# Kernel tuning notes

Measured on AMD Instinct MI355X. Metric: run time of the kernel, lower is better.

## Reference

```python
import jax, jax.numpy as jnp
import numpy as np

N = 50000       # nodes
E = 800000      # random edges (self-loops appended in reference)
F_IN = 3        # dataset.num_features
CH = 32         # conv_hidden_channels
HEADS = 4       # attention_heads
C1_OUT = CH * 2     # 64
C2_OUT = CH * 4     # 128
LIN = 256       # lin_hidden_channels
NCLS = 25       # dataset.num_classes


def setup_inputs() -> dict:
    key = jax.random.key(0)
    ks = jax.random.split(key, 20)
    g = lambda k, s: (jax.random.normal(k, s, jnp.float32) * 0.05)
    return {
        "x": jax.random.normal(ks[0], (N, F_IN), jnp.float32),
        "edge_index": jax.random.randint(ks[1], (2, E), 0, N, dtype=jnp.int64),
        # fc0 (Linear stored as [in, out])
        "fc0_w": g(ks[2], (F_IN, CH)), "fc0_b": g(ks[3], (CH,)),
        # FeaStConv 1: in=CH, out=C1_OUT
        "conv1_w": g(ks[4], (CH, HEADS * C1_OUT)),
        "conv1_u": g(ks[5], (CH, HEADS)),
        "conv1_c": g(ks[6], (HEADS,)),
        "conv1_b": g(ks[7], (C1_OUT,)),
        # FeaStConv 2: in=C1_OUT, out=C2_OUT
        "conv2_w": g(ks[8], (C1_OUT, HEADS * C2_OUT)),
        "conv2_u": g(ks[9], (C1_OUT, HEADS)),
        "conv2_c": g(ks[10], (HEADS,)),
        "conv2_b": g(ks[11], (C2_OUT,)),
        # fc1, fc2
        "fc1_w": g(ks[12], (C2_OUT, LIN)), "fc1_b": g(ks[13], (LIN,)),
        "fc2_w": g(ks[14], (LIN, NCLS)), "fc2_b": g(ks[15], (NCLS,)),
    }


def feast_conv(x, src, dst, W, u, c, b):
    """FeaStConv (PyG): q = softmax((x_j - x_i) u + c) over heads,
    msg = sum_h q_h * (x_j W_h), mean-aggregated onto dst nodes."""
    xi = x[dst]                          # [E', in]
    xj = x[src]                          # [E', in]
    q = jax.nn.softmax((xj - xi) @ u + c, axis=-1)   # [E', H]
    m = (xj @ W).reshape(xj.shape[0], HEADS, -1)     # [E', H, out]
    msg = jnp.einsum('eh,ehd->ed', q, m)             # [E', out]
    agg = jax.ops.segment_sum(msg, dst, num_segments=N)
    cnt = jax.ops.segment_sum(jnp.ones((msg.shape[0],), x.dtype), dst,
                              num_segments=N)
    return agg / cnt[:, None] + b


def reference(x, edge_index, fc0_w, fc0_b,
              conv1_w, conv1_u, conv1_c, conv1_b,
              conv2_w, conv2_u, conv2_c, conv2_b,
              fc1_w, fc1_b, fc2_w, fc2_b):
    loops = jnp.arange(N, dtype=edge_index.dtype)
    src = jnp.concatenate([edge_index[0], loops])   # messages flow src -> dst
    dst = jnp.concatenate([edge_index[1], loops])
    h = jax.nn.elu(x @ fc0_w + fc0_b)
    h = jax.nn.elu(feast_conv(h, src, dst, conv1_w, conv1_u, conv1_c, conv1_b))
    h = jax.nn.elu(feast_conv(h, src, dst, conv2_w, conv2_u, conv2_c, conv2_b))
    h = jax.nn.elu(h @ fc1_w + fc1_b)
    # dropout skipped (eval mode / training=self.training)
    out = h @ fc2_w + fc2_b
    return jax.nn.log_softmax(out, axis=1)
```

## Files before the change

kernel.cpp:

```cpp
#include <hip/hip_runtime.h>
#include <math.h>

#define F_IN 3
#define CH 32
#define HEADS 4
#define C1_OUT 64
#define C2_OUT 128
#define LIN 256
#define NCLS 25
#define NBIN 8

typedef __attribute__((ext_vector_type(8))) short bf16x8;
typedef __attribute__((ext_vector_type(4))) float f32x4;

__device__ __forceinline__ float elu_f(float x) {
    return x > 0.f ? x : (__expf(x) - 1.f);
}

__device__ __forceinline__ unsigned short f2bf(float f) {
    union { float f; unsigned int u; } v; v.f = f;
    unsigned int u = v.u + 0x7fffu + ((v.u >> 16) & 1u);
    return (unsigned short)(u >> 16);
}

__device__ __forceinline__ float bf2f(unsigned short u) {
    union { unsigned int u; float f; } v; v.u = ((unsigned int)u) << 16;
    return v.f;
}

__device__ __forceinline__ void unpackq(unsigned lo, unsigned hi, float& x, float& y,
                                        float& z, float& w) {
    x = bf2f((unsigned short)(lo & 0xffffu));
    y = bf2f((unsigned short)(lo >> 16));
    z = bf2f((unsigned short)(hi & 0xffffu));
    w = bf2f((unsigned short)(hi >> 16));
}

__device__ __forceinline__ void softmax4(const float* __restrict__ c,
                                         float& q0, float& q1, float& q2, float& q3) {
    float c0 = c[0], c1 = c[1], c2 = c[2], c3 = c[3];
    float mx = fmaxf(fmaxf(c0, c1), fmaxf(c2, c3));
    float e0 = __expf(c0 - mx), e1 = __expf(c1 - mx);
    float e2 = __expf(c2 - mx), e3 = __expf(c3 - mx);
    float inv = 1.f / (e0 + e1 + e2 + e3);
    q0 = e0 * inv; q1 = e1 * inv; q2 = e2 * inv; q3 = e3 * inv;
}

__device__ __forceinline__ void qslot(const float4* __restrict__ pp, float4 pd,
                                      float c0, float c1, float c2, float c3,
                                      int sx, bool valid,
                                      unsigned& qlo, unsigned& qhi) {
    float4 ps = pp[sx];
    float t0 = ps.x - pd.x + c0;
    float t1 = ps.y - pd.y + c1;
    float t2 = ps.z - pd.z + c2;
    float t3 = ps.w - pd.w + c3;
    float mx = fmaxf(fmaxf(t0, t1), fmaxf(t2, t3));
    float s0 = __expf(t0 - mx), s1 = __expf(t1 - mx);
    float s2 = __expf(t2 - mx), s3 = __expf(t3 - mx);
    float inv = 1.f / (s0 + s1 + s2 + s3);
    qlo = qhi = 0u;
    if (valid) {
        qlo = (unsigned)f2bf(s0 * inv) | ((unsigned)f2bf(s1 * inv) << 16);
        qhi = (unsigned)f2bf(s2 * inv) | ((unsigned)f2bf(s3 * inv) << 16);
    }
}

__global__ __launch_bounds__(256) void k_fc0(
    const float* __restrict__ x, const float* __restrict__ w,
    const float* __restrict__ b, const float* __restrict__ u,
    unsigned short* __restrict__ h0, float* __restrict__ p, int n_nodes) {
    int wid = (blockIdx.x * blockDim.x + threadIdx.x) >> 6;
    int lane = threadIdx.x & 63;
    int half = lane >> 5, c = lane & 31;
    int node = wid * 2 + half;
    if (node >= n_nodes) return;
    float acc = b[c];
#pragma unroll
    for (int i = 0; i < F_IN; ++i) acc += x[node * F_IN + i] * w[i * CH + c];
    unsigned short hb = f2bf(elu_f(acc));
    h0[(size_t)node * CH + c] = hb;
    float hv = bf2f(hb);
    float a0 = hv * u[c * HEADS + 0];
    float a1 = hv * u[c * HEADS + 1];
    float a2 = hv * u[c * HEADS + 2];
    float a3 = hv * u[c * HEADS + 3];
#pragma unroll
    for (int m = 16; m >= 1; m >>= 1) {
        a0 += __shfl_xor(a0, m, 32); a1 += __shfl_xor(a1, m, 32);
        a2 += __shfl_xor(a2, m, 32); a3 += __shfl_xor(a3, m, 32);
    }
    if (c == 0) {
        p[node * 4 + 0] = a0; p[node * 4 + 1] = a1;
        p[node * 4 + 2] = a2; p[node * 4 + 3] = a3;
    }
}

__global__ void k_deg(const int* __restrict__ dst, int* __restrict__ deg,
                      int ne, int npb) {
    int bin = blockIdx.x & (NBIN - 1);
    int blk = blockIdx.x >> 3;
    int nblk = gridDim.x >> 3;
    int per = (ne + nblk - 1) / nblk;
    int start = blk * per;
    int end = start + per < ne ? start + per : ne;
    int lo = bin * npb, hi = lo + npb;
    for (int e = start + threadIdx.x; e < end; e += blockDim.x) {
        int d = dst[e];
        if (d >= lo && d < hi) atomicAdd(&deg[d], 1);
    }
}

#define SCAN_BS 1024
__global__ __launch_bounds__(SCAN_BS) void k_scan_a(
    const int* __restrict__ deg, int* __restrict__ offa,
    int* __restrict__ blksum, int n) {
    __shared__ int buf[SCAN_BS];
    int tid = threadIdx.x;
    int i = blockIdx.x * SCAN_BS + tid;
    int v = (i < n) ? deg[i] : 0;
    buf[tid] = v;
    __syncthreads();
    for (int s = 1; s < SCAN_BS; s <<= 1) {
        int t = (tid >= s) ? buf[tid - s] : 0;
        __syncthreads();
        buf[tid] += t;
        __syncthreads();
    }
    if (i < n) offa[i] = buf[tid] - v;
    if (tid == SCAN_BS - 1) blksum[blockIdx.x] = buf[tid];
}

__global__ void k_scan_b(int* __restrict__ blksum, int* __restrict__ offa,
                         int nblk, int n) {
    int tid = threadIdx.x;
    int orig = (tid < nblk) ? blksum[tid] : 0;
    int v = orig;
#pragma unroll
    for (int s = 1; s < 64; s <<= 1) {
        int t = __shfl_up(v, s, 64);
        if (tid >= s) v += t;
    }
    if (tid < nblk) blksum[tid] = v - orig;
    if (tid == nblk - 1) offa[n] = v;
}

__global__ void k_scan_c(int* __restrict__ offa, int* __restrict__ cur,
                         const int* __restrict__ blksum, int n) {
    int i = blockIdx.x * blockDim.x + threadIdx.x;
    if (i < n) {
        int o = offa[i] + blksum[i >> 10];
        offa[i] = o;
        cur[i] = o;
    }
}

__global__ void k_scatter(const int* __restrict__ eidx, int* __restrict__ cur,
                          int2* __restrict__ ssd, int ne, int npb) {
    int bin = blockIdx.x & (NBIN - 1);
    int blk = blockIdx.x >> 3;
    int nblk = gridDim.x >> 3;
    int per = (ne + nblk - 1) / nblk;
    int start = blk * per;
    int end = start + per < ne ? start + per : ne;
    int lo = bin * npb, hi = lo + npb;
    for (int e = start + threadIdx.x; e < end; e += blockDim.x) {
        int d = eidx[ne + e];
        if (d >= lo && d < hi) {
            int s = eidx[e];
            int pos = atomicAdd(&cur[d], 1);
            ssd[pos] = make_int2(s, d);
        }
    }
}

template<int IN>
__global__ void k_proj(const unsigned short* __restrict__ h,
                       const float* __restrict__ u,
                       float* __restrict__ p, int n_nodes) {
    int node = blockIdx.x * blockDim.x + threadIdx.x;
    if (node >= n_nodes) return;
    const unsigned short* hr = h + (size_t)node * IN;
    float a0 = 0.f, a1 = 0.f, a2 = 0.f, a3 = 0.f;
#pragma unroll
    for (int kb = 0; kb < IN; kb += 8) {
        uint4 uu = *(const uint4*)(hr + kb);
        unsigned int ws_[4] = {uu.x, uu.y, uu.z, uu.w};
#pragma unroll
        for (int j = 0; j < 4; ++j) {
            float vlo = bf2f((unsigned short)(ws_[j] & 0xffffu));
            float vhi = bf2f((unsigned short)(ws_[j] >> 16));
            int k0 = kb + j * 2, k1 = kb + j * 2 + 1;
            a0 = fmaf(vlo, u[k0 * HEADS + 0], a0); a0 = fmaf(vhi, u[k1 * HEADS + 0], a0);
            a1 = fmaf(vlo, u[k0 * HEADS + 1], a1); a1 = fmaf(vhi, u[k1 * HEADS + 1], a1);
            a2 = fmaf(vlo, u[k0 * HEADS + 2], a2); a2 = fmaf(vhi, u[k1 * HEADS + 2], a2);
            a3 = fmaf(vlo, u[k0 * HEADS + 3], a3); a3 = fmaf(vhi, u[k1 * HEADS + 3], a3);
        }
    }
    p[node * 4 + 0] = a0; p[node * 4 + 1] = a1;
    p[node * 4 + 2] = a2; p[node * 4 + 3] = a3;
}

__global__ __launch_bounds__(256) void k_agg1(
    const unsigned short* __restrict__ h, const int* __restrict__ offa,
    const int2* __restrict__ ssd, const float* __restrict__ p,
    const float* __restrict__ cvec, unsigned short* __restrict__ arow,
    int n_nodes) {
    int wid = (blockIdx.x * blockDim.x + threadIdx.x) >> 6;
    int lane = threadIdx.x & 63;
    if (wid >= n_nodes) return;
    int half = lane >> 5, ch = lane & 31;
    int slot = lane & 7, sbase = lane & 56;
    int e0 = __builtin_amdgcn_readfirstlane(offa[wid]);
    int e1 = __builtin_amdgcn_readfirstlane(offa[wid + 1]);
    const float4* pp = (const float4*)p;
    float4 pd = pp[wid];
    float c0 = cvec[0], c1 = cvec[1], c2 = cvec[2], c3 = cvec[3];
    float a0 = 0.f, a1 = 0.f, a2 = 0.f, a3 = 0.f;
    for (int e = e0; e < e1; e += 8) {
        int ee = e + slot;
        int ec = ee < e1 ? ee : e0;
        int2 sd = ssd[ec];
        unsigned qlo, qhi;
        qslot(pp, pd, c0, c1, c2, c3, sd.x, ee < e1, qlo, qhi);
        int sx = sd.x;
#pragma unroll
        for (int m = 0; m < 4; ++m) {
            int src = sbase + 2 * m + half;
            int sj = __shfl(sx, src, 64);
            unsigned lo = (unsigned)__shfl((int)qlo, src, 64);
            unsigned hi = (unsigned)__shfl((int)qhi, src, 64);
            float xj = bf2f(h[(size_t)sj * CH + ch]);
            float qx, qy, qz, qw;
            unpackq(lo, hi, qx, qy, qz, qw);
            a0 = fmaf(qx, xj, a0); a1 = fmaf(qy, xj, a1);
            a2 = fmaf(qz, xj, a2); a3 = fmaf(qw, xj, a3);
        }
    }
    a0 += __shfl_xor(a0, 32); a1 += __shfl_xor(a1, 32);
    a2 += __shfl_xor(a2, 32); a3 += __shfl_xor(a3, 32);
    if (half == 0) {
        float qc0, qc1, qc2, qc3;
        softmax4(cvec, qc0, qc1, qc2, qc3);
        float xi = bf2f(h[(size_t)wid * CH + ch]);
        a0 = fmaf(qc0, xi, a0); a1 = fmaf(qc1, xi, a1);
        a2 = fmaf(qc2, xi, a2); a3 = fmaf(qc3, xi, a3);
        float inv = 1.f / (float)(e1 - e0 + 1);
        arow[(size_t)wid * 128 + 0 * CH + ch] = f2bf(a0 * inv);
        arow[(size_t)wid * 128 + 1 * CH + ch] = f2bf(a1 * inv);
        arow[(size_t)wid * 128 + 2 * CH + ch] = f2bf(a2 * inv);
        arow[(size_t)wid * 128 + 3 * CH + ch] = f2bf(a3 * inv);
    }
}

__global__ __launch_bounds__(256) void k_agg2(
    const unsigned short* __restrict__ h, const int* __restrict__ offa,
    const int2* __restrict__ ssd, const float* __restrict__ p,
    const float* __restrict__ cvec, unsigned short* __restrict__ arow,
    int n_nodes) {
    int wid = (blockIdx.x * blockDim.x + threadIdx.x) >> 6;
    int lane = threadIdx.x & 63;
    if (wid >= n_nodes) return;
    int slot = lane & 7, sbase = lane & 56;
    int e0 = __builtin_amdgcn_readfirstlane(offa[wid]);
    int e1 = __builtin_amdgcn_readfirstlane(offa[wid + 1]);
    const float4* pp = (const float4*)p;
    float4 pd = pp[wid];
    float c0 = cvec[0], c1 = cvec[1], c2 = cvec[2], c3 = cvec[3];
    float a0 = 0.f, a1 = 0.f, a2 = 0.f, a3 = 0.f;
    for (int e = e0; e < e1; e += 8) {
        int ee = e + slot;
        int ec = ee < e1 ? ee : e0;
        int2 sd = ssd[ec];
        unsigned qlo, qhi;
        qslot(pp, pd, c0, c1, c2, c3, sd.x, ee < e1, qlo, qhi);
        int sx = sd.x;
#pragma unroll
        for (int j = 0; j < 8; ++j) {
            int src = sbase + j;
            int sj = __shfl(sx, src, 64);
            unsigned lo = (unsigned)__shfl((int)qlo, src, 64);
            unsigned hi = (unsigned)__shfl((int)qhi, src, 64);
            float xj = bf2f(h[(size_t)sj * C1_OUT + lane]);
            float qx, qy, qz, qw;
            unpackq(lo, hi, qx, qy, qz, qw);
            a0 = fmaf(qx, xj, a0); a1 = fmaf(qy, xj, a1);
            a2 = fmaf(qz, xj, a2); a3 = fmaf(qw, xj, a3);
        }
    }
    float qc0, qc1, qc2, qc3;
    softmax4(cvec, qc0, qc1, qc2, qc3);
    float xi = bf2f(h[(size_t)wid * C1_OUT + lane]);
    a0 = fmaf(qc0, xi, a0); a1 = fmaf(qc1, xi, a1);
    a2 = fmaf(qc2, xi, a2); a3 = fmaf(qc3, xi, a3);
    float inv = 1.f / (float)(e1 - e0 + 1);
    arow[(size_t)wid * 256 + 0 * C1_OUT + lane] = f2bf(a0 * inv);
    arow[(size_t)wid * 256 + 1 * C1_OUT + lane] = f2bf(a1 * inv);
    arow[(size_t)wid * 256 + 2 * C1_OUT + lane] = f2bf(a2 * inv);
    arow[(size_t)wid * 256 + 3 * C1_OUT + lane] = f2bf(a3 * inv);
}

__global__ void k_prepAll(const float* __restrict__ W1, unsigned short* __restrict__ B1,
                          const float* __restrict__ W2, unsigned short* __restrict__ B2,
                          const float* __restrict__ Wf, unsigned short* __restrict__ Bf,
                          const float* __restrict__ Wc, unsigned short* __restrict__ Bc) {
    int idx = blockIdx.x * blockDim.x + threadIdx.x;
    if (idx < 8192) {
        int o = idx / 128, j = idx % 128;
        int hh = j / 32, k = j % 32;
        B1[idx] = f2bf(W1[k * (HEADS * 64) + hh * 64 + o]);
    } else if (idx < 40960) {
        int i = idx - 8192;
        int o = i / 256, j = i % 256;
        int hh = j / 64, k = j % 64;
        B2[i] = f2bf(W2[k * (HEADS * 128) + hh * 128 + o]);
    } else if (idx < 73728) {
        int i = idx - 40960;
        int o = i / 128, j = i % 128;
        Bf[i] = f2bf(Wf[j * 256 + o]);
    } else if (idx < 81920) {
        int i = idx - 73728;
        int o = i >> 8, k = i & 255;
        Bc[i] = f2bf(o < NCLS ? Wc[k * NCLS + o] : 0.f);
    }
}

template<int K, int M>
__global__ __launch_bounds__(256) void k_mgemm(
    const unsigned short* __restrict__ A, const unsigned short* __restrict__ Bt,
    const float* __restrict__ bias, unsigned short* __restrict__ D, int n) {
    constexpr int CPW = M / 4;
    constexpr int NCF = CPW / 16;
    constexpr int NKC = K / 32;
    __shared__ unsigned short Al[64 * K];
    int tid = threadIdx.x;
    int w = tid >> 6, l = tid & 63;
    int l16 = l & 15, l4 = l >> 4;
    int rowbase = blockIdx.x * 64;

    bf16x8 bfr[NCF][NKC];
#pragma unroll
    for (int c = 0; c < NCF; ++c)
#pragma unroll
        for (int t = 0; t < NKC; ++t) {
            int col = w * CPW + c * 16 + l16;
            int k = t * 32 + l4 * 8;
            bfr[c][t] = *(const bf16x8*)(Bt + (size_t)col * K + k);
        }

    constexpr int CHUNKS = 64 * K / 8;
    for (int idx = tid; idx < CHUNKS; idx += 256) {
        int row = idx / (K / 8);
        int kb = (idx % (K / 8)) * 8;
        int grow = rowbase + row;
        uint4 u;
        if (grow < n) u = *(const uint4*)(A + (size_t)grow * K + kb);
        else          u.x = u.y = u.z = u.w = 0u;
        int byte = ((row * K + kb) * 2) ^ ((row & 7) << 4);
        *(uint4*)((char*)Al + byte) = u;
    }
    __syncthreads();

#pragma unroll
    for (int r = 0; r < 4; ++r) {
        bf16x8 af[NKC];
        int row = r * 16 + l16;
#pragma unroll
        for (int t = 0; t < NKC; ++t) {
            int byte = ((row * K + t * 32 + l4 * 8) * 2) ^ ((row & 7) << 4);
            af[t] = *(bf16x8*)((char*)Al + byte);
        }
#pragma unroll
        for (int c = 0; c < NCF; ++c) {
            f32x4 acc = {0.f, 0.f, 0.f, 0.f};
#pragma unroll
            for (int t = 0; t < NKC; ++t)
                acc = __builtin_amdgcn_mfma_f32_16x16x32_bf16(af[t], bfr[c][t], acc, 0, 0, 0);
            int col = w * CPW + c * 16 + l16;
            float bv = bias[col];
#pragma unroll
            for (int j = 0; j < 4; ++j) {
                int grow = rowbase + r * 16 + l4 * 4 + j;
                if (grow < n)
                    D[(size_t)grow * M + col] = f2bf(elu_f(acc[j] + bv));
            }
        }
    }
}

__global__ __launch_bounds__(256) void k_fc2m(
    const unsigned short* __restrict__ A, const unsigned short* __restrict__ Bt,
    const float* __restrict__ bias, float* __restrict__ out, int n) {
    int tid = threadIdx.x;
    int w = tid >> 6, l = tid & 63;
    int l16 = l & 15, l4 = l >> 4;
    int rowbase = blockIdx.x * 256 + w * 64;

    bf16x8 bfr0[8], bfr1[8];
#pragma unroll
    for (int t = 0; t < 8; ++t) {
        int k = t * 32 + l4 * 8;
        bfr0[t] = *(const bf16x8*)(Bt + (size_t)l16 * LIN + k);
        bfr1[t] = *(const bf16x8*)(Bt + (size_t)(16 + l16) * LIN + k);
    }
    float b0 = bias[l16];
    bool hi_ok = (l16 < NCLS - 16);
    float b1 = hi_ok ? bias[16 + l16] : 0.f;

#pragma unroll
    for (int r = 0; r < 4; ++r) {
        int arow_i = rowbase + r * 16 + l16;
        int arc = arow_i < n ? arow_i : n - 1;
        const unsigned short* ar = A + (size_t)arc * LIN;
        bf16x8 af[8];
#pragma unroll
        for (int t = 0; t < 8; ++t)
            af[t] = *(const bf16x8*)(ar + t * 32 + l4 * 8);
        f32x4 acc0 = {0.f, 0.f, 0.f, 0.f}, acc1 = {0.f, 0.f, 0.f, 0.f};
#pragma unroll
        for (int t = 0; t < 8; ++t) {
            acc0 = __builtin_amdgcn_mfma_f32_16x16x32_bf16(af[t], bfr0[t], acc0, 0, 0, 0);
            acc1 = __builtin_amdgcn_mfma_f32_16x16x32_bf16(af[t], bfr1[t], acc1, 0, 0, 0);
        }
#pragma unroll
        for (int j = 0; j < 4; ++j) {
            float v0 = acc0[j] + b0;
            float v1 = acc1[j] + b1;
            float m = fmaxf(v0, hi_ok ? v1 : -1e30f);
#pragma unroll
            for (int msk = 8; msk >= 1; msk >>= 1)
                m = fmaxf(m, __shfl_xor(m, msk, 16));
            float s = __expf(v0 - m) + (hi_ok ? __expf(v1 - m) : 0.f);
#pragma unroll
            for (int msk = 8; msk >= 1; msk >>= 1)
                s += __shfl_xor(s, msk, 16);
            float lse = m + __logf(s);
            int ro = rowbase + r * 16 + l4 * 4 + j;
            if (ro < n) {
                out[(size_t)ro * NCLS + l16] = v0 - lse;
                if (hi_ok) out[(size_t)ro * NCLS + 16 + l16] = v1 - lse;
            }
        }
    }
}

extern "C" void kernel_launch(void* const* d_in, const int* in_sizes, int n_in,
                              void* d_out, int out_size, void* d_ws, size_t ws_size,
                              hipStream_t stream) {
    const float* x     = (const float*)d_in[0];
    const int*   eidx  = (const int*)d_in[1];
    const float* fc0_w = (const float*)d_in[2];
    const float* fc0_b = (const float*)d_in[3];
    const float* c1w   = (const float*)d_in[4];
    const float* c1u   = (const float*)d_in[5];
    const float* c1c   = (const float*)d_in[6];
    const float* c1b   = (const float*)d_in[7];
    const float* c2w   = (const float*)d_in[8];
    const float* c2u   = (const float*)d_in[9];
    const float* c2c   = (const float*)d_in[10];
    const float* c2b   = (const float*)d_in[11];
    const float* fc1w  = (const float*)d_in[12];
    const float* fc1b  = (const float*)d_in[13];
    const float* fc2w  = (const float*)d_in[14];
    const float* fc2b  = (const float*)d_in[15];

    int n_nodes = in_sizes[0] / F_IN;
    int ne      = in_sizes[1] / 2;

    auto align4 = [](size_t v) { return (v + 3) & ~(size_t)3; };
    float* ws = (float*)d_ws;
    size_t t = 0;
    size_t off_o = t; t += align4((size_t)n_nodes + 1);
    size_t cur_o = t; t += align4((size_t)n_nodes);
    size_t blk_o = t; t += 64;
    size_t p_o   = t; t += align4((size_t)n_nodes * 4);
    size_t h1_o  = t; t += align4((size_t)n_nodes * 32);
    size_t A_o   = t; t += align4((size_t)n_nodes * 128);
    size_t B_o   = t;
    size_t h0_o  = B_o;
    size_t ss_o  = align4(h0_o + (size_t)n_nodes * 16);
    size_t B_end = ss_o + (size_t)ne * 2;
    size_t B_sz  = B_end - B_o;
    size_t h2_sz = (size_t)n_nodes * 64;
    t = B_o + (B_sz > h2_sz ? B_sz : h2_sz);
    size_t bt1_o = t; t += 4096;
    size_t bt2_o = t; t += 16384;
    size_t btf_o = t; t += 16384;
    size_t btc_o = t; t += 4096;

    int*    offa   = (int*)(ws + off_o);
    int*    cur    = (int*)(ws + cur_o);
    int*    blksum = (int*)(ws + blk_o);
    float*  p      = ws + p_o;
    unsigned short* h1    = (unsigned short*)(ws + h1_o);
    unsigned short* arow1 = (unsigned short*)(ws + A_o);
    unsigned short* arow2 = (unsigned short*)(ws + A_o);
    unsigned short* h3    = (unsigned short*)(ws + A_o);
    unsigned short* h0    = (unsigned short*)(ws + h0_o);
    int2*   ssd    = (int2*)(ws + ss_o);
    unsigned short* h2    = (unsigned short*)(ws + B_o);
    unsigned short* bt1 = (unsigned short*)(ws + bt1_o);
    unsigned short* bt2 = (unsigned short*)(ws + bt2_o);
    unsigned short* btf = (unsigned short*)(ws + btf_o);
    unsigned short* btc = (unsigned short*)(ws + btc_o);
    float*  out    = (float*)d_out;

    int nblk = (n_nodes + SCAN_BS - 1) / SCAN_BS;
    int npb  = (n_nodes + NBIN - 1) / NBIN;

    hipMemsetAsync(cur, 0, (size_t)n_nodes * sizeof(int), stream);

    k_prepAll<<<(81920 + 255) / 256, 256, 0, stream>>>(c1w, bt1, c2w, bt2, fc1w, btf, fc2w, btc);

    k_fc0<<<(n_nodes * 32 + 255) / 256, 256, 0, stream>>>(x, fc0_w, fc0_b, c1u, h0, p, n_nodes);
    k_deg<<<NBIN * 512, 256, 0, stream>>>(eidx + ne, cur, ne, npb);
    k_scan_a<<<nblk, SCAN_BS, 0, stream>>>(cur, offa, blksum, n_nodes);
    k_scan_b<<<1, 64, 0, stream>>>(blksum, offa, nblk, n_nodes);
    k_scan_c<<<(n_nodes + 255) / 256, 256, 0, stream>>>(offa, cur, blksum, n_nodes);
    k_scatter<<<NBIN * 512, 256, 0, stream>>>(eidx, cur, ssd, ne, npb);

    int ngrid = (n_nodes + 63) / 64;

    k_agg1<<<(n_nodes * 64 + 255) / 256, 256, 0, stream>>>(h0, offa, ssd, p, c1c, arow1, n_nodes);
    k_mgemm<128, 64><<<ngrid, 256, 0, stream>>>(arow1, bt1, c1b, h1, n_nodes);

    k_proj<C1_OUT><<<(n_nodes + 255) / 256, 256, 0, stream>>>(h1, c2u, p, n_nodes);
    k_agg2<<<(n_nodes * 64 + 255) / 256, 256, 0, stream>>>(h1, offa, ssd, p, c2c, arow2, n_nodes);
    k_mgemm<256, 128><<<ngrid, 256, 0, stream>>>(arow2, bt2, c2b, h2, n_nodes);

    k_mgemm<128, 256><<<ngrid, 256, 0, stream>>>(h2, btf, fc1b, h3, n_nodes);
    k_fc2m<<<(n_nodes + 255) / 256, 256, 0, stream>>>(h3, btc, fc2b, out, n_nodes);
}
```

Baseline: 247.0 us.

## Fuse fc1 and fc2 into one head kernel and store only edge sources

The fc1 GEMM with ELU is fused with the fc2 GEMM and log-softmax into a single kernel. The 64x256 hidden tile stays in swizzled shared memory, so the h3 intermediate is never written to or read back from global memory. Separately, the sorted edge buffer now keeps only the source index instead of (src,dst) pairs, which halves scatter writes and aggregation reads. The fused kernel uses about 48KB of LDS per block, which may lower occupancy.

```diff
diff --git a/kernel.cpp b/kernel.cpp
--- a/kernel.cpp
+++ b/kernel.cpp
@@ -156,7 +156,7 @@
 }
 
 __global__ void k_scatter(const int* __restrict__ eidx, int* __restrict__ cur,
-                          int2* __restrict__ ssd, int ne, int npb) {
+                          int* __restrict__ ssrc, int ne, int npb) {
     int bin = blockIdx.x & (NBIN - 1);
     int blk = blockIdx.x >> 3;
     int nblk = gridDim.x >> 3;
@@ -169,7 +169,7 @@
         if (d >= lo && d < hi) {
             int s = eidx[e];
             int pos = atomicAdd(&cur[d], 1);
-            ssd[pos] = make_int2(s, d);
+            ssrc[pos] = s;
         }
     }
 }
@@ -203,7 +203,7 @@
 
 __global__ __launch_bounds__(256) void k_agg1(
     const unsigned short* __restrict__ h, const int* __restrict__ offa,
-    const int2* __restrict__ ssd, const float* __restrict__ p,
+    const int* __restrict__ ssrc, const float* __restrict__ p,
     const float* __restrict__ cvec, unsigned short* __restrict__ arow,
     int n_nodes) {
     int wid = (blockIdx.x * blockDim.x + threadIdx.x) >> 6;
@@ -220,10 +220,9 @@
     for (int e = e0; e < e1; e += 8) {
         int ee = e + slot;
         int ec = ee < e1 ? ee : e0;
-        int2 sd = ssd[ec];
+        int sx = ssrc[ec];
         unsigned qlo, qhi;
-        qslot(pp, pd, c0, c1, c2, c3, sd.x, ee < e1, qlo, qhi);
-        int sx = sd.x;
+        qslot(pp, pd, c0, c1, c2, c3, sx, ee < e1, qlo, qhi);
 #pragma unroll
         for (int m = 0; m < 4; ++m) {
             int src = sbase + 2 * m + half;
@@ -255,7 +254,7 @@
 
 __global__ __launch_bounds__(256) void k_agg2(
     const unsigned short* __restrict__ h, const int* __restrict__ offa,
-    const int2* __restrict__ ssd, const float* __restrict__ p,
+    const int* __restrict__ ssrc, const float* __restrict__ p,
     const float* __restrict__ cvec, unsigned short* __restrict__ arow,
     int n_nodes) {
     int wid = (blockIdx.x * blockDim.x + threadIdx.x) >> 6;
@@ -271,10 +270,9 @@
     for (int e = e0; e < e1; e += 8) {
         int ee = e + slot;
         int ec = ee < e1 ? ee : e0;
-        int2 sd = ssd[ec];
+        int sx = ssrc[ec];
         unsigned qlo, qhi;
-        qslot(pp, pd, c0, c1, c2, c3, sd.x, ee < e1, qlo, qhi);
-        int sx = sd.x;
+        qslot(pp, pd, c0, c1, c2, c3, sx, ee < e1, qlo, qhi);
 #pragma unroll
         for (int j = 0; j < 8; ++j) {
             int src = sbase + j;
@@ -388,58 +386,108 @@
     }
 }
 
-__global__ __launch_bounds__(256) void k_fc2m(
-    const unsigned short* __restrict__ A, const unsigned short* __restrict__ Bt,
-    const float* __restrict__ bias, float* __restrict__ out, int n) {
+__global__ __launch_bounds__(256) void k_head(
+    const unsigned short* __restrict__ A, const unsigned short* __restrict__ Btf,
+    const float* __restrict__ bias1, const unsigned short* __restrict__ Btc,
+    const float* __restrict__ bias2, float* __restrict__ out, int n) {
+    __shared__ unsigned short Al[64 * 128];
+    __shared__ unsigned short Hl[64 * 256];
     int tid = threadIdx.x;
     int w = tid >> 6, l = tid & 63;
     int l16 = l & 15, l4 = l >> 4;
-    int rowbase = blockIdx.x * 256 + w * 64;
-
-    bf16x8 bfr0[8], bfr1[8];
+    int rowbase = blockIdx.x * 64;
+
+    bf16x8 bfr[4][4];
+#pragma unroll
+    for (int c = 0; c < 4; ++c)
+#pragma unroll
+        for (int t = 0; t < 4; ++t) {
+            int col = w * 64 + c * 16 + l16;
+            int k = t * 32 + l4 * 8;
+            bfr[c][t] = *(const bf16x8*)(Btf + (size_t)col * 128 + k);
+        }
+
+    for (int idx = tid; idx < 1024; idx += 256) {
+        int row = idx >> 4;
+        int kb = (idx & 15) * 8;
+        int grow = rowbase + row;
+        uint4 u;
+        if (grow < n) u = *(const uint4*)(A + (size_t)grow * 128 + kb);
+        else          u.x = u.y = u.z = u.w = 0u;
+        int byte = ((row * 128 + kb) * 2) ^ ((row & 7) << 4);
+        *(uint4*)((char*)Al + byte) = u;
+    }
+    __syncthreads();
+
+#pragma unroll
+    for (int r = 0; r < 4; ++r) {
+        bf16x8 af[4];
+        int row = r * 16 + l16;
+#pragma unroll
+        for (int t = 0; t < 4; ++t) {
+            int byte = ((row * 128 + t * 32 + l4 * 8) * 2) ^ ((row & 7) << 4);
+            af[t] = *(bf16x8*)((char*)Al + byte);
+        }
+#pragma unroll
+        for (int c = 0; c < 4; ++c) {
+            f32x4 acc = {0.f, 0.f, 0.f, 0.f};
+#pragma unroll
+            for (int t = 0; t < 4; ++t)
+                acc = __builtin_amdgcn_mfma_f32_16x16x32_bf16(af[t], bfr[c][t], acc, 0, 0, 0);
+            int col = w * 64 + c * 16 + l16;
+            float bv = bias1[col];
+#pragma unroll
+            for (int j = 0; j < 4; ++j) {
+                int lrow = r * 16 + l4 * 4 + j;
+                unsigned short v = f2bf(elu_f(acc[j] + bv));
+                int byte = ((lrow * 256 + col) * 2) ^ ((lrow & 7) << 4);
+                *(unsigned short*)((char*)Hl + byte) = v;
+            }
+        }
+    }
+    __syncthreads();
+
+    bf16x8 b0[8], b1[8];
 #pragma unroll
     for (int t = 0; t < 8; ++t) {
         int k = t * 32 + l4 * 8;
-        bfr0[t] = *(const bf16x8*)(Bt + (size_t)l16 * LIN + k);
-        bfr1[t] = *(const bf16x8*)(Bt + (size_t)(16 + l16) * LIN + k);
-    }
-    float b0 = bias[l16];
+        b0[t] = *(const bf16x8*)(Btc + (size_t)l16 * LIN + k);
+        b1[t] = *(const bf16x8*)(Btc + (size_t)(16 + l16) * LIN + k);
+    }
+    float bb0 = bias2[l16];
     bool hi_ok = (l16 < NCLS - 16);
-    float b1 = hi_ok ? bias[16 + l16] : 0.f;
-
-#pragma unroll
-    for (int r = 0; r < 4; ++r) {
-        int arow_i = rowbase + r * 16 + l16;
-        int arc = arow_i < n ? arow_i : n - 1;
-        const unsigned short* ar = A + (size_t)arc * LIN;
-        bf16x8 af[8];
-#pragma unroll
-        for (int t = 0; t < 8; ++t)
-            af[t] = *(const bf16x8*)(ar + t * 32 + l4 * 8);
-        f32x4 acc0 = {0.f, 0.f, 0.f, 0.f}, acc1 = {0.f, 0.f, 0.f, 0.f};
-#pragma unroll
-        for (int t = 0; t < 8; ++t) {
-            acc0 = __builtin_amdgcn_mfma_f32_16x16x32_bf16(af[t], bfr0[t], acc0, 0, 0, 0);
-            acc1 = __builtin_amdgcn_mfma_f32_16x16x32_bf16(af[t], bfr1[t], acc1, 0, 0, 0);
-        }
-#pragma unroll
-        for (int j = 0; j < 4; ++j) {
-            float v0 = acc0[j] + b0;
-            float v1 = acc1[j] + b1;
-            float m = fmaxf(v0, hi_ok ? v1 : -1e30f);
-#pragma unroll
-            for (int msk = 8; msk >= 1; msk >>= 1)
-                m = fmaxf(m, __shfl_xor(m, msk, 16));
-            float s = __expf(v0 - m) + (hi_ok ? __expf(v1 - m) : 0.f);
-#pragma unroll
-            for (int msk = 8; msk >= 1; msk >>= 1)
-                s += __shfl_xor(s, msk, 16);
-            float lse = m + __logf(s);
-            int ro = rowbase + r * 16 + l4 * 4 + j;
-            if (ro < n) {
-                out[(size_t)ro * NCLS + l16] = v0 - lse;
-                if (hi_ok) out[(size_t)ro * NCLS + 16 + l16] = v1 - lse;
-            }
+    float bb1 = hi_ok ? bias2[16 + l16] : 0.f;
+
+    int lrow = w * 16 + l16;
+    bf16x8 af[8];
+#pragma unroll
+    for (int t = 0; t < 8; ++t) {
+        int byte = ((lrow * 256 + t * 32 + l4 * 8) * 2) ^ ((lrow & 7) << 4);
+        af[t] = *(bf16x8*)((char*)Hl + byte);
+    }
+    f32x4 acc0 = {0.f, 0.f, 0.f, 0.f}, acc1 = {0.f, 0.f, 0.f, 0.f};
+#pragma unroll
+    for (int t = 0; t < 8; ++t) {
+        acc0 = __builtin_amdgcn_mfma_f32_16x16x32_bf16(af[t], b0[t], acc0, 0, 0, 0);
+        acc1 = __builtin_amdgcn_mfma_f32_16x16x32_bf16(af[t], b1[t], acc1, 0, 0, 0);
+    }
+#pragma unroll
+    for (int j = 0; j < 4; ++j) {
+        float v0 = acc0[j] + bb0;
+        float v1 = acc1[j] + bb1;
+        float m = fmaxf(v0, hi_ok ? v1 : -1e30f);
+#pragma unroll
+        for (int msk = 8; msk >= 1; msk >>= 1)
+            m = fmaxf(m, __shfl_xor(m, msk, 16));
+        float s = __expf(v0 - m) + (hi_ok ? __expf(v1 - m) : 0.f);
+#pragma unroll
+        for (int msk = 8; msk >= 1; msk >>= 1)
+            s += __shfl_xor(s, msk, 16);
+        float lse = m + __logf(s);
+        int ro = rowbase + w * 16 + l4 * 4 + j;
+        if (ro < n) {
+            out[(size_t)ro * NCLS + l16] = v0 - lse;
+            if (hi_ok) out[(size_t)ro * NCLS + 16 + l16] = v1 - lse;
         }
     }
 }
@@ -479,7 +527,7 @@
     size_t B_o   = t;
     size_t h0_o  = B_o;
     size_t ss_o  = align4(h0_o + (size_t)n_nodes * 16);
-    size_t B_end = ss_o + (size_t)ne * 2;
+    size_t B_end = ss_o + (size_t)ne;
     size_t B_sz  = B_end - B_o;
     size_t h2_sz = (size_t)n_nodes * 64;
     t = B_o + (B_sz > h2_sz ? B_sz : h2_sz);
@@ -495,9 +543,8 @@
     unsigned short* h1    = (unsigned short*)(ws + h1_o);
     unsigned short* arow1 = (unsigned short*)(ws + A_o);
     unsigned short* arow2 = (unsigned short*)(ws + A_o);
-    unsigned short* h3    = (unsigned short*)(ws + A_o);
     unsigned short* h0    = (unsigned short*)(ws + h0_o);
-    int2*   ssd    = (int2*)(ws + ss_o);
+    int*    ssrc   = (int*)(ws + ss_o);
     unsigned short* h2    = (unsigned short*)(ws + B_o);
     unsigned short* bt1 = (unsigned short*)(ws + bt1_o);
     unsigned short* bt2 = (unsigned short*)(ws + bt2_o);
@@ -517,17 +564,16 @@
     k_scan_a<<<nblk, SCAN_BS, 0, stream>>>(cur, offa, blksum, n_nodes);
     k_scan_b<<<1, 64, 0, stream>>>(blksum, offa, nblk, n_nodes);
     k_scan_c<<<(n_nodes + 255) / 256, 256, 0, stream>>>(offa, cur, blksum, n_nodes);
-    k_scatter<<<NBIN * 512, 256, 0, stream>>>(eidx, cur, ssd, ne, npb);
+    k_scatter<<<NBIN * 512, 256, 0, stream>>>(eidx, cur, ssrc, ne, npb);
 
     int ngrid = (n_nodes + 63) / 64;
 
-    k_agg1<<<(n_nodes * 64 + 255) / 256, 256, 0, stream>>>(h0, offa, ssd, p, c1c, arow1, n_nodes);
+    k_agg1<<<(n_nodes * 64 + 255) / 256, 256, 0, stream>>>(h0, offa, ssrc, p, c1c, arow1, n_nodes);
     k_mgemm<128, 64><<<ngrid, 256, 0, stream>>>(arow1, bt1, c1b, h1, n_nodes);
 
     k_proj<C1_OUT><<<(n_nodes + 255) / 256, 256, 0, stream>>>(h1, c2u, p, n_nodes);
-    k_agg2<<<(n_nodes * 64 + 255) / 256, 256, 0, stream>>>(h1, offa, ssd, p, c2c, arow2, n_nodes);
+    k_agg2<<<(n_nodes * 64 + 255) / 256, 256, 0, stream>>>(h1, offa, ssrc, p, c2c, arow2, n_nodes);
     k_mgemm<256, 128><<<ngrid, 256, 0, stream>>>(arow2, bt2, c2b, h2, n_nodes);
 
-    k_mgemm<128, 256><<<ngrid, 256, 0, stream>>>(h2, btf, fc1b, h3, n_nodes);
-    k_fc2m<<<(n_nodes + 255) / 256, 256, 0, stream>>>(h3, btc, fc2b, out, n_nodes);
-}
+    k_head<<<ngrid, 256, 0, stream>>>(h2, btf, fc1b, btc, fc2b, out, n_nodes);
+}
```

Result: faster. 235.2 us (-4.8%).
